# Kernel optimization log

Measured on AMD Instinct MI355X. Metric: run time of the kernel, lower is better.

Reference implementation:

```python
import jax, jax.numpy as jnp
import numpy as np

B, S, D_MODEL = 1, 2048, 2048
H, KVH = 16, 4
HD = D_MODEL // H          # 128
N_REP = H // KVH           # 4 (GQA)
WINDOW = 1024              # window_size=(WINDOW-1, 0): self + 1023 past tokens
CLIP = 8.0
THETA = 500000.0
EPS = 1e-6
SCALE = 1.0 / (HD ** 0.5)


def rms_norm(x, w):
    # per-head RMSNorm over last dim (head_dim)
    var = jnp.mean(jnp.square(x), axis=-1, keepdims=True)
    return x * jax.lax.rsqrt(var + EPS) * w


def rope_tables():
    inv_freq = 1.0 / (THETA ** (jnp.arange(0, HD, 2, dtype=jnp.float32) / HD))
    pos = jnp.arange(S, dtype=jnp.float32)
    freqs = pos[:, None] * inv_freq[None, :]          # [S, HD/2]
    emb = jnp.concatenate([freqs, freqs], axis=-1)    # [S, HD]
    return jnp.cos(emb), jnp.sin(emb)


def rotate_half(x):
    x1, x2 = x[..., : HD // 2], x[..., HD // 2 :]
    return jnp.concatenate([-x2, x1], axis=-1)


def apply_rope(x, cos, sin):
    # x: [B, S, h, HD]; cos/sin: [S, HD]
    return x * cos[None, :, None, :] + rotate_half(x) * sin[None, :, None, :]


def setup_inputs() -> dict:
    key = jax.random.key(0)
    ks = jax.random.split(key, 7)
    w = lambda k, shape: jax.random.normal(k, shape, jnp.float32) * 0.02
    return {
        "x": jax.random.normal(ks[0], (B, S, D_MODEL), jnp.float32),
        "w_q": w(ks[1], (D_MODEL, D_MODEL)),
        "w_k": w(ks[2], (KVH * HD, D_MODEL)),
        "w_v": w(ks[3], (KVH * HD, D_MODEL)),
        "w_out": w(ks[4], (D_MODEL, D_MODEL)),
        "q_norm_w": jnp.ones((HD,), jnp.float32),
        "k_norm_w": jnp.ones((HD,), jnp.float32),
        "sinks": jax.random.normal(ks[5], (H,), jnp.float32),
    }


def reference(x, w_q, w_k, w_v, w_out, q_norm_w, k_norm_w, sinks):
    # fused QKV projection + clip
    q = jnp.clip(x @ w_q.T, -CLIP, CLIP).reshape(B, S, H, HD)
    k = jnp.clip(x @ w_k.T, -CLIP, CLIP).reshape(B, S, KVH, HD)
    v = jnp.clip(x @ w_v.T, -CLIP, CLIP).reshape(B, S, KVH, HD)

    # per-head qk RMSNorm, then RoPE
    q = rms_norm(q, q_norm_w)
    k = rms_norm(k, k_norm_w)
    cos, sin = rope_tables()
    q = apply_rope(q, cos, sin)
    k = apply_rope(k, cos, sin)

    # GQA: repeat_interleave kv heads
    k = jnp.repeat(k, N_REP, axis=2)  # [B, S, H, HD]
    v = jnp.repeat(v, N_REP, axis=2)

    # sliding-window causal attention with a learned per-head sink logit
    logits = jnp.einsum("bqhd,bkhd->bhqk", q, k) * SCALE  # [B, H, S, S]
    qi = jnp.arange(S)[:, None]
    ki = jnp.arange(S)[None, :]
    mask = (ki <= qi) & (ki > qi - WINDOW)                # causal + window
    logits = jnp.where(mask[None, None, :, :], logits, -jnp.inf)

    # sink token: always-visible extra logit sinks[h] with zero value vector
    sink_col = jnp.broadcast_to(sinks[None, :, None, None], (B, H, S, 1))
    full = jnp.concatenate([logits, sink_col], axis=-1)   # [B, H, S, S+1]
    probs = jax.nn.softmax(full, axis=-1)

    att = jnp.einsum("bhqk,bkhd->bqhd", probs[..., :S], v)  # sink value is 0
    return att.reshape(B, S, D_MODEL) @ w_out.T
```

## Files before the change

kernel.cpp:

```cpp
#include <hip/hip_runtime.h>
#include <hip/hip_bf16.h>
#include <math.h>

#define S_LEN 2048
#define DMODEL 2048
#define NH 16
#define NKVH 4
#define HDIM 128
#define WINDOW 1024

typedef __bf16 bf16;
typedef __bf16 bf16x8 __attribute__((ext_vector_type(8)));
typedef __bf16 bf16x4 __attribute__((ext_vector_type(4)));
typedef float floatx4 __attribute__((ext_vector_type(4)));

static __device__ __forceinline__ bf16x8 load_bf8(const bf16* p) {
    return *reinterpret_cast<const bf16x8*>(p);
}

static __device__ __forceinline__ void async16(const bf16* g, bf16* l) {
    __builtin_amdgcn_global_load_lds(
        (const __attribute__((address_space(1))) void*)g,
        (__attribute__((address_space(3))) void*)l, 16, 0, 0);
}

__global__ __launch_bounds__(256) void convert_kernel(
    const float* __restrict__ x, const float* __restrict__ wq,
    const float* __restrict__ wk, const float* __restrict__ wv,
    const float* __restrict__ wo,
    bf16* __restrict__ xb, bf16* __restrict__ wqb, bf16* __restrict__ wkb,
    bf16* __restrict__ wvb, bf16* __restrict__ wob) {
    int i = blockIdx.x * blockDim.x + threadIdx.x;
    const float* src; bf16* dst; int off;
    if      (i < 1048576) { src = x;  dst = xb;  off = i; }
    else if (i < 2097152) { src = wq; dst = wqb; off = i - 1048576; }
    else if (i < 2359296) { src = wk; dst = wkb; off = i - 2097152; }
    else if (i < 2621440) { src = wv; dst = wvb; off = i - 2359296; }
    else if (i < 3670016) { src = wo; dst = wob; off = i - 2621440; }
    else return;
    float4 v = reinterpret_cast<const float4*>(src)[off];
    union { bf16 b[4]; ushort4 u; } t;
    t.b[0] = (bf16)v.x; t.b[1] = (bf16)v.y; t.b[2] = (bf16)v.z; t.b[3] = (bf16)v.w;
    reinterpret_cast<ushort4*>(dst)[off] = t.u;
}

#define GEMM_BODY(EXTRA_LDS_DECLS)                                             \
    __shared__ __align__(16) bf16 smem[2 * (64 + 128) * 64];        \
    EXTRA_LDS_DECLS                                                            \
    int tid = threadIdx.x;                                                     \
    int lane = tid & 63, wid = tid >> 6;                                       \
    int l15 = lane & 15, quad = lane >> 4;                                     \
    int rlocal = lane >> 3;                                                    \
    int scol = ((lane & 7) ^ rlocal) * 8;                                      \
    const bf16* gA = A + (size_t)(m0 + wid * 16 + rlocal) * K + scol;          \
    const bf16* gB = B + (size_t)(n0 + wid * 32 + rlocal) * K + scol;          \
    int ldsOfA = (wid * 16) * 64;                                               \
    int ldsOfB = (wid * 32) * 64;                                               \
    floatx4 acc[2][4];                                                         \
    _Pragma("unroll") for (int mi = 0; mi < 2; ++mi)                           \
        _Pragma("unroll") for (int ni = 0; ni < 4; ++ni)                       \
            acc[mi][ni] = floatx4{0.f, 0.f, 0.f, 0.f};                         \
    int mb = (wid & 1) * 32, nb = (wid >> 1) * 64;                             \
    _Pragma("unroll") for (int j = 0; j < 2; ++j)                              \
        async16(gA + (size_t)(j * 8) * K, smem + ldsOfA + j * 512);            \
    _Pragma("unroll") for (int j = 0; j < 4; ++j)                              \
        async16(gB + (size_t)(j * 8) * K, smem + 8192 + ldsOfB + j * 512);     \
    int buf = 0;                                                               \
    for (int k0 = 0; k0 < K; k0 += 64) {                                       \
        __syncthreads();                                                       \
        if (k0 + 64 < K) {                                                     \
            int nof = buf ^ 1;                                                 \
            _Pragma("unroll") for (int j = 0; j < 2; ++j)                      \
                async16(gA + (size_t)(j * 8) * K + k0 + 64,                    \
                        smem + nof * 4096 + ldsOfA + j * 512);                 \
            _Pragma("unroll") for (int j = 0; j < 4; ++j)                      \
                async16(gB + (size_t)(j * 8) * K + k0 + 64,                    \
                        smem + 8192 + nof * 8192 + ldsOfB + j * 512);          \
        }                                                                      \
        const bf16* sA = smem + buf * 4096;                                    \
        const bf16* sB = smem + 8192 + buf * 8192;                             \
        _Pragma("unroll") for (int kc = 0; kc < 2; ++kc) {                     \
            bf16x8 af[2], bq[4];                                               \
            int ch = ((kc << 2) + quad) ^ (l15 & 7);                           \
            _Pragma("unroll") for (int i = 0; i < 2; ++i)                      \
                af[i] = load_bf8(sA + (mb + i * 16 + l15) * 64 + ch * 8);      \
            _Pragma("unroll") for (int i = 0; i < 4; ++i)                      \
                bq[i] = load_bf8(sB + (nb + i * 16 + l15) * 64 + ch * 8);      \
            _Pragma("unroll") for (int mi = 0; mi < 2; ++mi)                   \
                _Pragma("unroll") for (int ni = 0; ni < 4; ++ni)               \
                    acc[mi][ni] = __builtin_amdgcn_mfma_f32_16x16x32_bf16(     \
                        af[mi], bq[ni], acc[mi][ni], 0, 0, 0);                 \
        }                                                                      \
        buf ^= 1;                                                              \
    }

__global__ __launch_bounds__(256) void gemm_qkv_fused(
    const bf16* __restrict__ A, const bf16* __restrict__ B,
    const float* __restrict__ qw, const float* __restrict__ kw,
    bf16* __restrict__ qb, bf16* __restrict__ kb, bf16* __restrict__ vtb) {
    const int K = 2048;
    int m0 = blockIdx.y * 64, n0 = blockIdx.x * 128;
    GEMM_BODY(__shared__ float rowss[64][2];)

#pragma unroll
    for (int mi = 0; mi < 2; ++mi)
#pragma unroll
        for (int ni = 0; ni < 4; ++ni)
#pragma unroll
            for (int r = 0; r < 4; ++r)
                acc[mi][ni][r] = fminf(fmaxf(acc[mi][ni][r], -8.0f), 8.0f);

    if (n0 >= 2560) {
#pragma unroll
        for (int mi = 0; mi < 2; ++mi)
#pragma unroll
            for (int ni = 0; ni < 4; ++ni)
#pragma unroll
                for (int r = 0; r < 4; ++r) {
                    int row = m0 + mb + mi * 16 + quad * 4 + r;
                    int n = n0 + nb + ni * 16 + l15;
                    vtb[(size_t)(n - 2560) * 2048 + row] = (bf16)acc[mi][ni][r];
                }
        return;
    }

    __syncthreads();
    bf16 (*xnorm)[128] = (bf16(*)[128])(smem + 8192);

#pragma unroll
    for (int mi = 0; mi < 2; ++mi)
#pragma unroll
        for (int r = 0; r < 4; ++r) {
            float s = 0.f;
#pragma unroll
            for (int ni = 0; ni < 4; ++ni) s += acc[mi][ni][r] * acc[mi][ni][r];
#pragma unroll
            for (int o = 1; o < 16; o <<= 1) s += __shfl_xor(s, o, 64);
            if (l15 == 0) rowss[mb + mi * 16 + quad * 4 + r][wid >> 1] = s;
        }
    __syncthreads();

    const float* nw = (n0 < 2048) ? qw : kw;
#pragma unroll
    for (int mi = 0; mi < 2; ++mi)
#pragma unroll
        for (int r = 0; r < 4; ++r) {
            int row = mb + mi * 16 + quad * 4 + r;
            float var = (rowss[row][0] + rowss[row][1]) * (1.0f / 128.0f);
            float rinv = rsqrtf(var + 1e-6f);
#pragma unroll
            for (int ni = 0; ni < 4; ++ni) {
                int col = nb + ni * 16 + l15;
                float xn = acc[mi][ni][r] * rinv * nw[col];
                acc[mi][ni][r] = xn;
                xnorm[row][col] = (bf16)xn;
            }
        }
    __syncthreads();

    float invf[4];
#pragma unroll
    for (int ni = 0; ni < 4; ++ni) {
        int fi = (nb + ni * 16 + l15) & 63;
        invf[ni] = __expf((float)fi * (-13.122363377404328f / 64.0f));
    }
    bool lowhalf = (nb == 0);
#pragma unroll
    for (int mi = 0; mi < 2; ++mi)
#pragma unroll
        for (int r = 0; r < 4; ++r) {
            int row = mb + mi * 16 + quad * 4 + r;
            float pos = (float)(m0 + row);
#pragma unroll
            for (int ni = 0; ni < 4; ++ni) {
                int col = nb + ni * 16 + l15;
                float ang = pos * invf[ni];
                float c = __cosf(ang), sn = __sinf(ang);
                float part = (float)xnorm[row][col ^ 64];
                float rot = lowhalf ? -part : part;
                float o = acc[mi][ni][r] * c + rot * sn;
                int n = n0 + col;
                int s = m0 + row;
                if (n0 < 2048) qb[(size_t)s * 2048 + n] = (bf16)o;
                else           kb[(size_t)s * 512 + (n - 2048)] = (bf16)o;
            }
        }
}

__global__ __launch_bounds__(256) void gemm_out(
    const bf16* __restrict__ A, const bf16* __restrict__ B,
    float* __restrict__ C) {
    const int K = 2048, N = 2048;
    int m0 = blockIdx.y * 64, n0 = blockIdx.x * 128;
    GEMM_BODY()
#pragma unroll
    for (int mi = 0; mi < 2; ++mi)
#pragma unroll
        for (int ni = 0; ni < 4; ++ni)
#pragma unroll
            for (int r = 0; r < 4; ++r) {
                int m = m0 + mb + mi * 16 + quad * 4 + r;
                int n = n0 + nb + ni * 16 + l15;
                C[(size_t)m * N + n] = acc[mi][ni][r];
            }
}

__global__ __launch_bounds__(256) void attn(
    const bf16* __restrict__ qb, const bf16* __restrict__ kb,
    const bf16* __restrict__ vtb, const float* __restrict__ sinks,
    bf16* __restrict__ attb) {
    __shared__ __align__(16) bf16 sK[2][64 * 128];
    __shared__ __align__(16) bf16 sV[2][128 * 64];
    __shared__ __align__(16) bf16 sP[64 * 72];
    __shared__ float redu[64][4];
    int tid = threadIdx.x;
    int lane = tid & 63, wid = tid >> 6;
    int l15 = lane & 15, quad = lane >> 4;
    int h = blockIdx.y, kh = h >> 2;
    int bq0 = blockIdx.x * 64;

    bf16x8 qf[4][4];
#pragma unroll
    for (int ni = 0; ni < 4; ++ni) {
        const bf16* qrow = qb + (size_t)(bq0 + ni * 16 + l15) * 2048 + h * 128 + quad * 8;
#pragma unroll
        for (int kc = 0; kc < 4; ++kc) qf[ni][kc] = load_bf8(qrow + kc * 32);
    }

    floatx4 acc[4][2];
#pragma unroll
    for (int mi = 0; mi < 4; ++mi)
#pragma unroll
        for (int df = 0; df < 2; ++df) acc[mi][df] = floatx4{0.f, 0.f, 0.f, 0.f};
    float lpq[4];
#pragma unroll
    for (int ni = 0; ni < 4; ++ni) lpq[ni] = 0.f;

    int keyit = wid * 4 + (lane >> 4);
    int gcK = (lane & 15) ^ keyit;
    int dimit = wid * 8 + (lane >> 3);
    int gcV = (lane & 7) ^ ((lane >> 3) & 7);

    int tstart = bq0 - 1024; if (tstart < 0) tstart = 0;
    const bf16* kbase = kb + (size_t)kh * 128;
    const bf16* vbase = vtb + (size_t)kh * 128 * 2048;

#pragma unroll
    for (int r = 0; r < 4; ++r) {
        async16(kbase + (size_t)(tstart + r * 16 + keyit) * 512 + gcK * 8,
                sK[0] + (r * 16 + wid * 4) * 128);
        async16(vbase + (size_t)(r * 32 + dimit) * 2048 + tstart + gcV * 8,
                sV[0] + (r * 32 + wid * 8) * 64);
    }

    int buf = 0;
    for (int t = tstart; t <= bq0; t += 64) {
        __syncthreads();
        if (t + 64 <= bq0) {
#pragma unroll
            for (int r = 0; r < 4; ++r) {
                async16(kbase + (size_t)(t + 64 + r * 16 + keyit) * 512 + gcK * 8,
                        sK[buf ^ 1] + (r * 16 + wid * 4) * 128);
                async16(vbase + (size_t)(r * 32 + dimit) * 2048 + t + 64 + gcV * 8,
                        sV[buf ^ 1] + (r * 32 + wid * 8) * 64);
            }
        }
        floatx4 ST[4];
#pragma unroll
        for (int ni = 0; ni < 4; ++ni) ST[ni] = floatx4{0.f, 0.f, 0.f, 0.f};
#pragma unroll
        for (int kc = 0; kc < 4; ++kc) {
            int ch = (kc * 4 + quad) ^ l15;
            bf16x8 kf = load_bf8(sK[buf] + (wid * 16 + l15) * 128 + ch * 8);
#pragma unroll
            for (int ni = 0; ni < 4; ++ni)
                ST[ni] = __builtin_amdgcn_mfma_f32_16x16x32_bf16(kf, qf[ni][kc], ST[ni], 0, 0, 0);
        }
        int kbi = t + wid * 16 + quad * 4;
#pragma unroll
        for (int ni = 0; ni < 4; ++ni) {
            int qi = bq0 + ni * 16 + l15;
            bf16x4 pv;
#pragma unroll
            for (int r = 0; r < 4; ++r) {
                int ki = kbi + r;
                float v = ST[ni][r] * 0.08838834764831845f;
                bool ok = (ki <= qi) && (ki > qi - WINDOW);
                float e = ok ? __expf(v) : 0.0f;
                lpq[ni] += e;
                pv[r] = (bf16)e;
            }
            *(bf16x4*)(sP + (ni * 16 + l15) * 72 + wid * 16 + quad * 4) = pv;
        }
        __syncthreads();
#pragma unroll
        for (int kc = 0; kc < 2; ++kc) {
            bf16x8 pf[4];
#pragma unroll
            for (int mi = 0; mi < 4; ++mi)
                pf[mi] = load_bf8(sP + (mi * 16 + l15) * 72 + kc * 32 + quad * 8);
#pragma unroll
            for (int df = 0; df < 2; ++df) {
                int dim = wid * 32 + df * 16 + l15;
                int ch = (kc * 4 + quad) ^ (l15 & 7);
                bf16x8 vf = load_bf8(sV[buf] + dim * 64 + ch * 8);
#pragma unroll
                for (int mi = 0; mi < 4; ++mi)
                    acc[mi][df] = __builtin_amdgcn_mfma_f32_16x16x32_bf16(pf[mi], vf, acc[mi][df], 0, 0, 0);
            }
        }
        buf ^= 1;
    }

#pragma unroll
    for (int ni = 0; ni < 4; ++ni) {
        float v = lpq[ni];
        v += __shfl_xor(v, 16, 64);
        v += __shfl_xor(v, 32, 64);
        if (quad == 0) redu[ni * 16 + l15][wid] = v;
    }
    __syncthreads();
    float sk = __expf(sinks[h]);
#pragma unroll
    for (int mi = 0; mi < 4; ++mi)
#pragma unroll
        for (int r = 0; r < 4; ++r) {
            int row = mi * 16 + quad * 4 + r;
            float rs = redu[row][0] + redu[row][1] + redu[row][2] + redu[row][3] + sk;
            float inv = 1.0f / rs;
#pragma unroll
            for (int df = 0; df < 2; ++df) {
                int dim = wid * 32 + df * 16 + l15;
                attb[(size_t)(bq0 + row) * 2048 + h * 128 + dim] =
                    (bf16)(acc[mi][df][r] * inv);
            }
        }
}

extern "C" void kernel_launch(void* const* d_in, const int* in_sizes, int n_in,
                              void* d_out, int out_size, void* d_ws, size_t ws_size,
                              hipStream_t stream) {
    const float* x      = (const float*)d_in[0];
    const float* w_q    = (const float*)d_in[1];
    const float* w_k    = (const float*)d_in[2];
    const float* w_v    = (const float*)d_in[3];
    const float* w_out  = (const float*)d_in[4];
    const float* q_norm = (const float*)d_in[5];
    const float* k_norm = (const float*)d_in[6];
    const float* sinks  = (const float*)d_in[7];

    char* ws = (char*)d_ws;
    const size_t MB = 1u << 20;
    bf16* xb   = (bf16*)(ws + 0 * MB);
    bf16* wqb  = (bf16*)(ws + 8 * MB);
    bf16* wkb  = (bf16*)(ws + 16 * MB);
    bf16* wvb  = (bf16*)(ws + 18 * MB);
    bf16* wob  = (bf16*)(ws + 20 * MB);
    bf16* qb   = (bf16*)(ws + 28 * MB);
    bf16* kb   = (bf16*)(ws + 36 * MB);
    bf16* vtb  = (bf16*)(ws + 38 * MB);
    bf16* attb = (bf16*)(ws + 40 * MB);
    bf16* wcomb = wqb;
    float* out = (float*)d_out;

    convert_kernel<<<14336, 256, 0, stream>>>(x, w_q, w_k, w_v, w_out,
                                              xb, wqb, wkb, wvb, wob);
    gemm_qkv_fused<<<dim3(24, 32), 256, 0, stream>>>(xb, wcomb, q_norm, k_norm,
                                                     qb, kb, vtb);
    attn<<<dim3(32, 16), 256, 0, stream>>>(qb, kb, vtb, sinks, attb);
    gemm_out<<<dim3(16, 32), 256, 0, stream>>>(attb, wob, out);
}
```

Before: 205.4 us.

## Enlarge QKV GEMM tile to 128x256 and do norm/RoPE in registers

```diff
diff --git a/kernel.cpp b/kernel.cpp
--- a/kernel.cpp
+++ b/kernel.cpp
@@ -30,23 +30,24 @@
     const float* __restrict__ wo,
     bf16* __restrict__ xb, bf16* __restrict__ wqb, bf16* __restrict__ wkb,
     bf16* __restrict__ wvb, bf16* __restrict__ wob) {
-    int i = blockIdx.x * blockDim.x + threadIdx.x;
-    const float* src; bf16* dst; int off;
-    if      (i < 1048576) { src = x;  dst = xb;  off = i; }
-    else if (i < 2097152) { src = wq; dst = wqb; off = i - 1048576; }
-    else if (i < 2359296) { src = wk; dst = wkb; off = i - 2097152; }
-    else if (i < 2621440) { src = wv; dst = wvb; off = i - 2359296; }
-    else if (i < 3670016) { src = wo; dst = wob; off = i - 2621440; }
-    else return;
-    float4 v = reinterpret_cast<const float4*>(src)[off];
-    union { bf16 b[4]; ushort4 u; } t;
-    t.b[0] = (bf16)v.x; t.b[1] = (bf16)v.y; t.b[2] = (bf16)v.z; t.b[3] = (bf16)v.w;
-    reinterpret_cast<ushort4*>(dst)[off] = t.u;
-}
-
-#define GEMM_BODY(EXTRA_LDS_DECLS)                                             \
+    for (int i = blockIdx.x * blockDim.x + threadIdx.x; i < 3670016;
+         i += gridDim.x * blockDim.x) {
+        const float* src; bf16* dst; int off;
+        if      (i < 1048576) { src = x;  dst = xb;  off = i; }
+        else if (i < 2097152) { src = wq; dst = wqb; off = i - 1048576; }
+        else if (i < 2359296) { src = wk; dst = wkb; off = i - 2097152; }
+        else if (i < 2621440) { src = wv; dst = wvb; off = i - 2359296; }
+        else                  { src = wo; dst = wob; off = i - 2621440; }
+        float4 v = reinterpret_cast<const float4*>(src)[off];
+        union { bf16 b[4]; ushort4 u; } t;
+        t.b[0] = (bf16)v.x; t.b[1] = (bf16)v.y;
+        t.b[2] = (bf16)v.z; t.b[3] = (bf16)v.w;
+        reinterpret_cast<ushort4*>(dst)[off] = t.u;
+    }
+}
+
+#define GEMM_BODY()                                                            \
     __shared__ __align__(16) bf16 smem[2 * (64 + 128) * 64];        \
-    EXTRA_LDS_DECLS                                                            \
     int tid = threadIdx.x;                                                     \
     int lane = tid & 63, wid = tid >> 6;                                       \
     int l15 = lane & 15, quad = lane >> 4;                                     \
@@ -94,27 +95,84 @@
         buf ^= 1;                                                              \
     }
 
-__global__ __launch_bounds__(256) void gemm_qkv_fused(
+__global__ __launch_bounds__(256, 1) void gemm_qkv_fused(
     const bf16* __restrict__ A, const bf16* __restrict__ B,
     const float* __restrict__ qw, const float* __restrict__ kw,
     bf16* __restrict__ qb, bf16* __restrict__ kb, bf16* __restrict__ vtb) {
     const int K = 2048;
-    int m0 = blockIdx.y * 64, n0 = blockIdx.x * 128;
-    GEMM_BODY(__shared__ float rowss[64][2];)
-
-#pragma unroll
-    for (int mi = 0; mi < 2; ++mi)
-#pragma unroll
-        for (int ni = 0; ni < 4; ++ni)
+    int m0 = blockIdx.y * 128, n0 = blockIdx.x * 256;
+    __shared__ __align__(16) bf16 smem[2 * 24576];
+    int tid = threadIdx.x;
+    int lane = tid & 63, wid = tid >> 6;
+    int l15 = lane & 15, quad = lane >> 4;
+    int rlocal = lane >> 3;
+    int scol = ((lane & 7) ^ rlocal) * 8;
+    const bf16* gA = A + (size_t)(m0 + wid * 32 + rlocal) * K + scol;
+    const bf16* gB = B + (size_t)(n0 + wid * 64 + rlocal) * K + scol;
+    int mb = (wid & 1) * 64, nb = (wid >> 1) * 128;
+
+    floatx4 acc[4][8];
+#pragma unroll
+    for (int mi = 0; mi < 4; ++mi)
+#pragma unroll
+        for (int ni = 0; ni < 8; ++ni) acc[mi][ni] = floatx4{0.f, 0.f, 0.f, 0.f};
+
+#pragma unroll
+    for (int j = 0; j < 4; ++j)
+        async16(gA + (size_t)(j * 8) * K, smem + (wid * 32 + j * 8) * 64);
+#pragma unroll
+    for (int j = 0; j < 8; ++j)
+        async16(gB + (size_t)(j * 8) * K, smem + 8192 + (wid * 64 + j * 8) * 64);
+
+    int buf = 0;
+    for (int k0 = 0; k0 < K; k0 += 64) {
+        __syncthreads();
+        if (k0 + 64 < K) {
+            bf16* nbase = smem + (buf ^ 1) * 24576;
+#pragma unroll
+            for (int j = 0; j < 4; ++j)
+                async16(gA + (size_t)(j * 8) * K + k0 + 64,
+                        nbase + (wid * 32 + j * 8) * 64);
+#pragma unroll
+            for (int j = 0; j < 8; ++j)
+                async16(gB + (size_t)(j * 8) * K + k0 + 64,
+                        nbase + 8192 + (wid * 64 + j * 8) * 64);
+        }
+        const bf16* sA = smem + buf * 24576;
+        const bf16* sB = sA + 8192;
+#pragma unroll
+        for (int kc = 0; kc < 2; ++kc) {
+            bf16x8 af[4], bq[8];
+            int ch = ((kc << 2) + quad) ^ (l15 & 7);
+#pragma unroll
+            for (int i = 0; i < 4; ++i)
+                af[i] = load_bf8(sA + (mb + i * 16 + l15) * 64 + ch * 8);
+#pragma unroll
+            for (int n = 0; n < 8; ++n)
+                bq[n] = load_bf8(sB + (nb + n * 16 + l15) * 64 + ch * 8);
+#pragma unroll
+            for (int mi = 0; mi < 4; ++mi)
+#pragma unroll
+                for (int ni = 0; ni < 8; ++ni)
+                    acc[mi][ni] = __builtin_amdgcn_mfma_f32_16x16x32_bf16(
+                        af[mi], bq[ni], acc[mi][ni], 0, 0, 0);
+        }
+        buf ^= 1;
+    }
+
+#pragma unroll
+    for (int mi = 0; mi < 4; ++mi)
+#pragma unroll
+        for (int ni = 0; ni < 8; ++ni)
 #pragma unroll
             for (int r = 0; r < 4; ++r)
                 acc[mi][ni][r] = fminf(fmaxf(acc[mi][ni][r], -8.0f), 8.0f);
 
     if (n0 >= 2560) {
 #pragma unroll
-        for (int mi = 0; mi < 2; ++mi)
-#pragma unroll
-            for (int ni = 0; ni < 4; ++ni)
+        for (int mi = 0; mi < 4; ++mi)
+#pragma unroll
+            for (int ni = 0; ni < 8; ++ni)
 #pragma unroll
                 for (int r = 0; r < 4; ++r) {
                     int row = m0 + mb + mi * 16 + quad * 4 + r;
@@ -124,65 +182,52 @@
         return;
     }
 
-    __syncthreads();
-    bf16 (*xnorm)[128] = (bf16(*)[128])(smem + 8192);
-
-#pragma unroll
-    for (int mi = 0; mi < 2; ++mi)
+    const float* nw = (n0 < 2048) ? qw : kw;
+    float nwv[8];
+#pragma unroll
+    for (int ni = 0; ni < 8; ++ni) nwv[ni] = nw[(nb + ni * 16 + l15) & 127];
+#pragma unroll
+    for (int mi = 0; mi < 4; ++mi)
 #pragma unroll
         for (int r = 0; r < 4; ++r) {
             float s = 0.f;
 #pragma unroll
-            for (int ni = 0; ni < 4; ++ni) s += acc[mi][ni][r] * acc[mi][ni][r];
+            for (int ni = 0; ni < 8; ++ni) s += acc[mi][ni][r] * acc[mi][ni][r];
 #pragma unroll
             for (int o = 1; o < 16; o <<= 1) s += __shfl_xor(s, o, 64);
-            if (l15 == 0) rowss[mb + mi * 16 + quad * 4 + r][wid >> 1] = s;
-        }
-    __syncthreads();
-
-    const float* nw = (n0 < 2048) ? qw : kw;
-#pragma unroll
-    for (int mi = 0; mi < 2; ++mi)
+            float rinv = rsqrtf(s * (1.0f / 128.0f) + 1e-6f);
+#pragma unroll
+            for (int ni = 0; ni < 8; ++ni) acc[mi][ni][r] *= rinv * nwv[ni];
+        }
+
+    float invf[4];
+#pragma unroll
+    for (int ni = 0; ni < 4; ++ni) {
+        int fi = ni * 16 + l15;
+        invf[ni] = __expf((float)fi * (-13.122363377404328f / 64.0f));
+    }
+#pragma unroll
+    for (int mi = 0; mi < 4; ++mi)
 #pragma unroll
         for (int r = 0; r < 4; ++r) {
             int row = mb + mi * 16 + quad * 4 + r;
-            float var = (rowss[row][0] + rowss[row][1]) * (1.0f / 128.0f);
-            float rinv = rsqrtf(var + 1e-6f);
+            int s = m0 + row;
+            float pos = (float)s;
 #pragma unroll
             for (int ni = 0; ni < 4; ++ni) {
-                int col = nb + ni * 16 + l15;
-                float xn = acc[mi][ni][r] * rinv * nw[col];
-                acc[mi][ni][r] = xn;
-                xnorm[row][col] = (bf16)xn;
-            }
-        }
-    __syncthreads();
-
-    float invf[4];
-#pragma unroll
-    for (int ni = 0; ni < 4; ++ni) {
-        int fi = (nb + ni * 16 + l15) & 63;
-        invf[ni] = __expf((float)fi * (-13.122363377404328f / 64.0f));
-    }
-    bool lowhalf = (nb == 0);
-#pragma unroll
-    for (int mi = 0; mi < 2; ++mi)
-#pragma unroll
-        for (int r = 0; r < 4; ++r) {
-            int row = mb + mi * 16 + quad * 4 + r;
-            float pos = (float)(m0 + row);
-#pragma unroll
-            for (int ni = 0; ni < 4; ++ni) {
-                int col = nb + ni * 16 + l15;
                 float ang = pos * invf[ni];
                 float c = __cosf(ang), sn = __sinf(ang);
-                float part = (float)xnorm[row][col ^ 64];
-                float rot = lowhalf ? -part : part;
-                float o = acc[mi][ni][r] * c + rot * sn;
-                int n = n0 + col;
-                int s = m0 + row;
-                if (n0 < 2048) qb[(size_t)s * 2048 + n] = (bf16)o;
-                else           kb[(size_t)s * 512 + (n - 2048)] = (bf16)o;
+                float a = acc[mi][ni][r], b2 = acc[mi][ni + 4][r];
+                float olo = a * c - b2 * sn;
+                float ohi = b2 * c + a * sn;
+                int nlo = n0 + nb + ni * 16 + l15;
+                if (n0 < 2048) {
+                    qb[(size_t)s * 2048 + nlo] = (bf16)olo;
+                    qb[(size_t)s * 2048 + nlo + 64] = (bf16)ohi;
+                } else {
+                    kb[(size_t)s * 512 + (nlo - 2048)] = (bf16)olo;
+                    kb[(size_t)s * 512 + (nlo - 2048) + 64] = (bf16)ohi;
+                }
             }
         }
 }
@@ -363,9 +408,9 @@
     bf16* wcomb = wqb;
     float* out = (float*)d_out;
 
-    convert_kernel<<<14336, 256, 0, stream>>>(x, w_q, w_k, w_v, w_out,
-                                              xb, wqb, wkb, wvb, wob);
-    gemm_qkv_fused<<<dim3(24, 32), 256, 0, stream>>>(xb, wcomb, q_norm, k_norm,
+    convert_kernel<<<2048, 256, 0, stream>>>(x, w_q, w_k, w_v, w_out,
+                                             xb, wqb, wkb, wvb, wob);
+    gemm_qkv_fused<<<dim3(12, 16), 256, 0, stream>>>(xb, wcomb, q_norm, k_norm,
                                                      qb, kb, vtb);
     attn<<<dim3(32, 16), 256, 0, stream>>>(qb, kb, vtb, sinks, attb);
     gemm_out<<<dim3(16, 32), 256, 0, stream>>>(attb, wob, out);
```

Result: no change. 202.2 us (-1.6%).
